# Performance work log

Measured on AMD Instinct MI355X. Metric: run time of the kernel, lower is better.

Reference implementation:

```python
import jax, jax.numpy as jnp
import numpy as np

B, NQ, NC, D, H, HD, FF, RB = 2, 512, 2048, 768, 12, 64, 3072, 64
EPS = 1e-5


def setup_inputs() -> dict:
    key = jax.random.key(0)
    ks = jax.random.split(key, 20)
    def n(k, shape, s=0.02):
        return jax.random.normal(k, shape, jnp.float32) * s
    return dict(
        query_state=n(ks[0], (B, NQ, D), 1.0),
        context_k=n(ks[1], (B, NC, D), 1.0),
        context_v=n(ks[2], (B, NC, D), 1.0),
        query_coords=jax.random.uniform(ks[3], (B, NQ, 2), jnp.float32),
        context_coords=jax.random.uniform(ks[4], (B, NC, 2), jnp.float32),
        sn_g=jnp.ones(D), sn_b=jnp.zeros(D),
        wqkv=n(ks[5], (D, 3 * D)), bqkv=jnp.zeros(3 * D),
        wo_s=n(ks[6], (D, D)), bo_s=jnp.zeros(D),
        cn_g=jnp.ones(D), cn_b=jnp.zeros(D),
        wq=n(ks[7], (D, D)), bq=jnp.zeros(D),
        wk=n(ks[8], (D, D)), bk=jnp.zeros(D),
        wv=n(ks[9], (D, D)), bv=jnp.zeros(D),
        wo_c=n(ks[10], (D, D)), bo_c=jnp.zeros(D),
        rb_w1=n(ks[11], (2, RB), 0.5), rb_b1=jnp.zeros(RB),
        rb_w2=n(ks[12], (RB, H), 0.5), rb_b2=jnp.zeros(H),
        fn_g=jnp.ones(D), fn_b=jnp.zeros(D),
        fw1=n(ks[13], (D, FF)), fb1=jnp.zeros(FF),
        fw2=n(ks[14], (FF, D)), fb2=jnp.zeros(D),
    )


def _ln(x, g, b):
    m = x.mean(-1, keepdims=True)
    v = ((x - m) ** 2).mean(-1, keepdims=True)
    return (x - m) / jnp.sqrt(v + EPS) * g + b


def _heads(x):
    # (B, N, D) -> (B, H, N, HD)
    return x.reshape(x.shape[0], x.shape[1], H, HD).transpose(0, 2, 1, 3)


def reference(query_state, context_k, context_v, query_coords, context_coords,
              sn_g, sn_b, wqkv, bqkv, wo_s, bo_s,
              cn_g, cn_b, wq, bq, wk, bk, wv, bv, wo_c, bo_c,
              rb_w1, rb_b1, rb_w2, rb_b2,
              fn_g, fn_b, fw1, fb1, fw2, fb2):
    scale = HD ** -0.5
    x = query_state

    # ---- pre-norm self-attention (nn.MultiheadAttention equivalent) ----
    qn = _ln(x, sn_g, sn_b)
    qkv = qn @ wqkv + bqkv                      # (B, NQ, 3D)
    q, k, v = jnp.split(qkv, 3, axis=-1)
    q, k, v = _heads(q), _heads(k), _heads(v)   # (B, H, NQ, HD)
    a = jax.nn.softmax(jnp.einsum('bhqd,bhkd->bhqk', q, k) * scale, axis=-1)
    o = jnp.einsum('bhqk,bhkd->bhqd', a, v).transpose(0, 2, 1, 3).reshape(B, NQ, D)
    x = x + o @ wo_s + bo_s

    # ---- relative coordinate bias: MLP(delta) -> (B, H, NQ, NC) ----
    delta = query_coords[:, :, None, :] - context_coords[:, None, :, :]  # (B, NQ, NC, 2)
    bias = jax.nn.gelu(delta @ rb_w1 + rb_b1, approximate=False) @ rb_w2 + rb_b2
    bias = bias.transpose(0, 3, 1, 2)           # (B, H, NQ, NC)

    # ---- pre-norm cross-attention with bias ----
    qn = _ln(x, cn_g, cn_b)
    q = _heads(qn @ wq + bq)                    # (B, H, NQ, HD)
    k = _heads(context_k @ wk + bk)             # (B, H, NC, HD)
    v = _heads(context_v @ wv + bv)
    logits = jnp.einsum('bhqd,bhkd->bhqk', q, k) * scale + bias
    a = jax.nn.softmax(logits, axis=-1)
    o = jnp.einsum('bhqk,bhkd->bhqd', a, v).transpose(0, 2, 1, 3).reshape(B, NQ, D)
    x = x + o @ wo_c + bo_c

    # ---- pre-norm FFN ----
    h = jax.nn.gelu(_ln(x, fn_g, fn_b) @ fw1 + fb1, approximate=False)
    x = x + h @ fw2 + fb2
    return x
```

## Files before the change

kernel.cpp:

```cpp
#include <hip/hip_runtime.h>

#define B_ 2
#define NQ_ 512
#define NC_ 2048
#define D_ 768
#define H_ 12
#define HD_ 64
#define FF_ 3072
#define RB_ 64

typedef unsigned short u16;
typedef __attribute__((ext_vector_type(4))) unsigned short u16x4;
typedef __attribute__((ext_vector_type(8))) short short8;
typedef __attribute__((ext_vector_type(4))) float f32x4;
typedef __attribute__((ext_vector_type(2))) float f32x2;

#define SCL2 0.18033688f

__device__ __forceinline__ float bf2f(u16 u) {
    unsigned int i = ((unsigned int)u) << 16;
    float f; __builtin_memcpy(&f, &i, 4); return f;
}
__device__ __forceinline__ u16 f2bf(float f) {
    unsigned int i; __builtin_memcpy(&i, &f, 4);
    unsigned int r = i + 0x7FFFu + ((i >> 16) & 1u);
    return (u16)(r >> 16);
}
__device__ __forceinline__ float gelu_f(float x) {
    return 0.5f * x * (1.f + erff(x * 0.70710678118654752f));
}
__device__ __forceinline__ float wsum(float v) {
    v += __shfl_xor(v, 32); v += __shfl_xor(v, 16); v += __shfl_xor(v, 8);
    v += __shfl_xor(v, 4);  v += __shfl_xor(v, 2);  v += __shfl_xor(v, 1);
    return v;
}
__device__ __forceinline__ void gload_lds16(const void* g, void* l) {
    __builtin_amdgcn_global_load_lds((const __attribute__((address_space(1))) void*)g,
                                     (__attribute__((address_space(3))) void*)l, 16, 0, 0);
}

__device__ __forceinline__ void wtrans_body(const float* __restrict__ in, u16* __restrict__ out,
                                            int K, int N, int bx, int by, int tid) {
    __shared__ float t[32][33];
    int n0 = bx * 32, k0 = by * 32;
    int tx = tid & 31, ty = tid >> 5;
#pragma unroll
    for (int r = 0; r < 4; ++r)
        t[ty + r * 8][tx] = in[(long)(k0 + ty + r * 8) * N + n0 + tx];
    __syncthreads();
#pragma unroll
    for (int r = 0; r < 4; ++r)
        out[(long)(n0 + ty + r * 8) * K + k0 + tx] = f2bf(t[tx][ty + r * 8]);
}

__global__ __launch_bounds__(256) void prep(
    const float* wqkv, u16* wT_qkv,
    const float* wo_s, const float* wq, const float* wk, const float* wv, const float* wo_c,
    u16* wT_os, u16* wT_q, u16* wT_k, u16* wT_v, u16* wT_oc,
    const float* fw1, u16* wT_f1, const float* fw2, u16* wT_f2,
    const float* ctx_k, u16* ckb, const float* ctx_v, u16* cvb,
    const float* bk, const float* bv, float* bkv) {
    int i = blockIdx.x, tid = threadIdx.x;
    if (i < 1728) { wtrans_body(wqkv, wT_qkv, 768, 2304, i % 72, i / 72, tid); return; }
    i -= 1728;
    if (i < 2880) {
        int z = i / 576, rem = i % 576;
        const float* in; u16* out;
        switch (z) {
            case 0: in = wo_s; out = wT_os; break;
            case 1: in = wq;   out = wT_q;  break;
            case 2: in = wk;   out = wT_k;  break;
            case 3: in = wv;   out = wT_v;  break;
            default: in = wo_c; out = wT_oc; break;
        }
        wtrans_body(in, out, 768, 768, rem % 24, rem / 24, tid);
        return;
    }
    i -= 2880;
    if (i < 2304) { wtrans_body(fw1, wT_f1, 768, 3072, i % 96, i / 96, tid); return; }
    i -= 2304;
    if (i < 2304) { wtrans_body(fw2, wT_f2, 3072, 768, i % 24, i / 24, tid); return; }
    i -= 2304;
    if (i < 6144) {
        int y = i / 3072;
        int ii = (i % 3072) * 256 + tid;
        const float* in = y ? ctx_v : ctx_k;
        u16* out = y ? cvb : ckb;
        float4 v = ((const float4*)in)[ii];
        u16x4 o; o.x = f2bf(v.x); o.y = f2bf(v.y); o.z = f2bf(v.z); o.w = f2bf(v.w);
        ((u16x4*)out)[ii] = o;
        return;
    }
    i -= 6144;
    {
        int j = i * 256 + tid;
        if (j < 768) bkv[j] = bk[j];
        else if (j < 1536) bkv[j] = bv[j - 768];
    }
}

__global__ __launch_bounds__(256) void ln_k(const float* __restrict__ x, const float* __restrict__ g,
                                            const float* __restrict__ bta, u16* __restrict__ out) {
    int row = blockIdx.x, t = threadIdx.x;
    const float* xr = x + (long)row * D_;
    float a0 = xr[t], a1 = xr[t + 256], a2 = xr[t + 512];
    float s = a0 + a1 + a2, s2 = a0 * a0 + a1 * a1 + a2 * a2;
    s = wsum(s); s2 = wsum(s2);
    __shared__ float rb[8];
    int lane = t & 63, wid = t >> 6;
    if (!lane) { rb[wid] = s; rb[wid + 4] = s2; }
    __syncthreads();
    float S = rb[0] + rb[1] + rb[2] + rb[3];
    float S2 = rb[4] + rb[5] + rb[6] + rb[7];
    float mean = S * (1.f / D_);
    float var = S2 * (1.f / D_) - mean * mean;
    float rstd = rsqrtf(var + 1e-5f);
    u16* orow = out + (long)row * D_;
    orow[t]       = f2bf((a0 - mean) * rstd * g[t]       + bta[t]);
    orow[t + 256] = f2bf((a1 - mean) * rstd * g[t + 256] + bta[t + 256]);
    orow[t + 512] = f2bf((a2 - mean) * rstd * g[t + 512] + bta[t + 512]);
}

#define BIAS_SMEM_BYTES (5888 + 12 * 264 * 2)
__device__ __forceinline__ void bias_body(char* smem,
    const float* __restrict__ qcoord, const float* __restrict__ ccoord,
    const float* __restrict__ w1, const float* __restrict__ b1,
    const float* __restrict__ w2, const float* __restrict__ b2,
    u16* __restrict__ out, int cx, int q4, int b, int tid) {
    float* s1 = (float*)smem;
    float* sw2 = (float*)(smem + 768);
    float2* sc = (float2*)(smem + 3840);
    u16* sb = (u16*)(smem + 5888);
    int q0 = q4 * 4, c0 = cx * 256;
    if (tid < 64) { s1[tid] = w1[tid]; s1[64 + tid] = w1[64 + tid]; s1[128 + tid] = b1[tid]; }
    for (int i = tid; i < RB_ * H_; i += 256) sw2[i] = w2[i];
    sc[tid] = ((const float2*)ccoord)[b * NC_ + c0 + tid];
    __syncthreads();
    int lane = tid & 63, wid = tid >> 6;
    int h = lane & 15, g4 = lane >> 4;
    int j0 = g4 * 8;
    f32x2 wx[8], wy[8], bb[8];
#pragma unroll
    for (int p = 0; p < 4; ++p) {
        wx[p]     = (f32x2){s1[j0 + 2 * p],       s1[j0 + 2 * p + 1]};
        wy[p]     = (f32x2){s1[64 + j0 + 2 * p],  s1[64 + j0 + 2 * p + 1]};
        bb[p]     = (f32x2){s1[128 + j0 + 2 * p], s1[128 + j0 + 2 * p + 1]};
        wx[4 + p] = (f32x2){s1[32 + j0 + 2 * p],  s1[32 + j0 + 2 * p + 1]};
        wy[4 + p] = (f32x2){s1[96 + j0 + 2 * p],  s1[96 + j0 + 2 * p + 1]};
        bb[4 + p] = (f32x2){s1[160 + j0 + 2 * p], s1[160 + j0 + 2 * p + 1]};
    }
    short8 vb0, vb1;
#pragma unroll
    for (int u = 0; u < 8; ++u) {
        vb0[u] = (h < 12) ? (short)f2bf(sw2[(j0 + u) * H_ + h]) : (short)0;
        vb1[u] = (h < 12) ? (short)f2bf(sw2[(32 + j0 + u) * H_ + h]) : (short)0;
    }
    float qx[4], qy[4];
#pragma unroll
    for (int qq = 0; qq < 4; ++qq) {
        qx[qq] = qcoord[(b * NQ_ + q0 + qq) * 2];
        qy[qq] = qcoord[(b * NQ_ + q0 + qq) * 2 + 1];
    }
    float b2v = (h < 12) ? b2[h] : 0.f;
#pragma unroll 1
    for (int qq = 0; qq < 4; ++qq) {
        if (qq) __syncthreads();
#pragma unroll
        for (int it = 0; it < 4; ++it) {
            int ci = wid * 64 + it * 16 + h;
            float2 cc = sc[ci];
            float dx = qx[qq] - cc.x, dy = qy[qq] - cc.y;
            unsigned int pk[8];
#pragma unroll
            for (int p = 0; p < 8; ++p) {
                f32x2 pre = dx * wx[p] + bb[p];
                pre = dy * wy[p] + pre;
                f32x2 xc = __builtin_elementwise_min(
                               __builtin_elementwise_max(pre, (f32x2)(-3.0f)), (f32x2)(3.0f));
                f32x2 u = xc * xc;
                f32x2 v = u * 2.3813e-5f + (-6.8939e-4f);
                v = v * u + 0.0086261f;
                v = v * u + (-0.064949f);
                v = v * u + 0.39837f;
                f32x2 phi = xc * v + 0.5f;
                f32x2 g = pre * phi;
                pk[p] = __builtin_amdgcn_perm(__builtin_bit_cast(unsigned int, g.y),
                                              __builtin_bit_cast(unsigned int, g.x), 0x07060302u);
            }
            uint4 d0 = {pk[0], pk[1], pk[2], pk[3]};
            uint4 d1 = {pk[4], pk[5], pk[6], pk[7]};
            short8 a0 = __builtin_bit_cast(short8, d0);
            short8 a1 = __builtin_bit_cast(short8, d1);
            f32x4 acc = {};
            acc = __builtin_amdgcn_mfma_f32_16x16x32_bf16(a0, vb0, acc, 0, 0, 0);
            acc = __builtin_amdgcn_mfma_f32_16x16x32_bf16(a1, vb1, acc, 0, 0, 0);
            if (h < 12) {
#pragma unroll
                for (int r = 0; r < 4; ++r) {
                    int loc = wid * 64 + it * 16 + g4 * 4 + r;
                    sb[h * 264 + loc] = f2bf((acc[r] + b2v) * 1.4426950f);
                }
            }
        }
        __syncthreads();
        for (int i = tid; i < 12 * 128; i += 256) {
            int row = i >> 7, cp = (i & 127) * 2;
            unsigned int pv = *(const unsigned int*)(sb + row * 264 + cp);
            *(unsigned int*)(out + (((long)(b * H_ + row) * NQ_ + q0 + qq) * NC_ + c0 + cp)) = pv;
        }
    }
}

__global__ __launch_bounds__(256) void vtrans(const u16* __restrict__ in, u16* __restrict__ out,
                                              int NCt, int ldin, int bdiv, long sIb, long sIh) {
    __shared__ u16 t[32][33];
    int z = blockIdx.z, zb = z / bdiv, zh = z % bdiv;
    const u16* ib = in + zb * sIb + zh * sIh;
    int c0 = blockIdx.x * 32, d0 = blockIdx.y * 32;
    int tx = threadIdx.x & 31, ty = threadIdx.x >> 5;
#pragma unroll
    for (int r = 0; r < 4; ++r)
        t[ty + r * 8][tx] = ib[(long)(c0 + ty + r * 8) * ldin + d0 + tx];
    __syncthreads();
#pragma unroll
    for (int r = 0; r < 4; ++r)
        out[(long)z * 64 * NCt + (long)(d0 + ty + r * 8) * NCt + c0 + tx] = t[tx][ty + r * 8];
}

template <int NCT, bool HASBIAS>
__global__ __launch_bounds__(64) void fattn(
    const u16* __restrict__ Qb, const u16* __restrict__ Kb, const u16* __restrict__ Vtb,
    const u16* __restrict__ Bias, u16* __restrict__ Ob, int ldq, int ldk) {
    __shared__ u16 kl[2][128 * 64];
    __shared__ u16 vl[64 * 128];
    __shared__ u16 pl[16 * 128];
    const int lane = threadIdx.x;
    const int h16 = lane & 15, g4 = lane >> 4;
    const int hh = blockIdx.y, b = blockIdx.z, q0 = blockIdx.x * 16;
    const u16* Qrow = Qb + (long)(b * NQ_ + q0 + h16) * ldq + hh * 64;
    short8 qf0 = *(const short8*)(Qrow + g4 * 8);
    short8 qf1 = *(const short8*)(Qrow + 32 + g4 * 8);
    const u16* Kbase = Kb + (long)b * NCT * ldk + hh * 64;
    const u16* Vtbase = Vtb + (long)(b * H_ + hh) * 64 * NCT;

    auto stageK = [&](int buf, int c0) {
#pragma unroll
        for (int i = 0; i < 16; ++i) {
            int ch = i * 64 + lane;
            int row = ch >> 3, col2 = (ch & 7) * 16;
            int scol2 = col2 ^ ((row & 7) << 4);
            gload_lds16(Kbase + (long)(c0 + row) * ldk + (scol2 >> 1), &kl[buf][ch * 8]);
        }
    };
    auto stageV = [&](int c0) {
#pragma unroll
        for (int i = 0; i < 16; ++i) {
            int ch = i * 64 + lane;
            int row = ch >> 4, col2 = (ch & 15) * 16;
            int scol2 = col2 ^ ((row & 15) << 4);
            gload_lds16(Vtbase + (long)row * NCT + c0 + (scol2 >> 1), &vl[ch * 8]);
        }
    };

    float m0[4] = {-1e30f, -1e30f, -1e30f, -1e30f};
    float l0[4] = {0.f, 0.f, 0.f, 0.f};
    f32x4 oacc[4] = {};
    constexpr int T = NCT / 128;
    stageK(0, 0);
    for (int t = 0; t < T; ++t) {
        const int c0 = t * 128, cur = t & 1;
        asm volatile("s_waitcnt lgkmcnt(0)" ::: "memory");
        stageV(c0);
        if (t + 1 < T) stageK(cur ^ 1, c0 + 128);
        if (t + 1 < T) asm volatile("s_waitcnt vmcnt(32)" ::: "memory");
        else           asm volatile("s_waitcnt vmcnt(16)" ::: "memory");
        f32x4 sacc[8] = {};
        const u16* klc = kl[cur];
        __builtin_amdgcn_s_setprio(1);
#pragma unroll
        for (int n = 0; n < 8; ++n) {
            int row = n * 16 + h16, swz = (row & 7) << 4;
#pragma unroll
            for (int ks = 0; ks < 2; ++ks) {
                short8 kf = *(const short8*)((const char*)klc + row * 128 + ((ks * 64 + g4 * 16) ^ swz));
                sacc[n] = __builtin_amdgcn_mfma_f32_16x16x32_bf16(ks ? qf1 : qf0, kf, sacc[n], 0, 0, 0);
            }
        }
        __builtin_amdgcn_s_setprio(0);
        if (t + 1 < T) asm volatile("s_waitcnt vmcnt(16)" ::: "memory");
        else           asm volatile("s_waitcnt vmcnt(0)" ::: "memory");
        float cr[4];
#pragma unroll
        for (int r = 0; r < 4; ++r) {
            float mx = -1e30f;
#pragma unroll
            for (int n = 0; n < 8; ++n) {
                float s = sacc[n][r] * SCL2;
                sacc[n][r] = s; mx = fmaxf(mx, s);
            }
            mx = fmaxf(mx, __shfl_xor(mx, 1)); mx = fmaxf(mx, __shfl_xor(mx, 2));
            mx = fmaxf(mx, __shfl_xor(mx, 4)); mx = fmaxf(mx, __shfl_xor(mx, 8));
            float mn = fmaxf(m0[r], mx);
            cr[r] = __builtin_amdgcn_exp2f(m0[r] - mn); m0[r] = mn;
            float sum = 0.f;
#pragma unroll
            for (int n = 0; n < 8; ++n) {
                float p = __builtin_amdgcn_exp2f(sacc[n][r] - mn); sacc[n][r] = p; sum += p;
            }
            sum += __shfl_xor(sum, 1); sum += __shfl_xor(sum, 2);
            sum += __shfl_xor(sum, 4); sum += __shfl_xor(sum, 8);
            l0[r] = l0[r] * cr[r] + sum;
        }
#pragma unroll
        for (int n = 0; n < 8; ++n)
#pragma unroll
            for (int r = 0; r < 4; ++r) {
                int q = g4 * 4 + r, c = n * 16 + h16;
                *(u16*)((char*)pl + q * 256 + ((c * 2) ^ (q << 4))) =
                    (u16)(__builtin_bit_cast(unsigned int, sacc[n][r]) >> 16);
            }
#pragma unroll
        for (int d = 0; d < 4; ++d) {
            f32x4 o = oacc[d];
            o[0] *= cr[0]; o[1] *= cr[1]; o[2] *= cr[2]; o[3] *= cr[3];
            oacc[d] = o;
        }
        short8 pf[4];
#pragma unroll
        for (int ks = 0; ks < 4; ++ks)
            pf[ks] = *(const short8*)((const char*)pl + h16 * 256 + ((ks * 64 + g4 * 16) ^ (h16 << 4)));
        __builtin_amdgcn_s_setprio(1);
#pragma unroll
        for (int d = 0; d < 4; ++d) {
            int row = d * 16 + h16, swzv = (row & 15) << 4;
#pragma unroll
            for (int ks = 0; ks < 4; ++ks) {
                short8 vf = *(const short8*)((const char*)vl + row * 256 + ((ks * 64 + g4 * 16) ^ swzv));
                oacc[d] = __builtin_amdgcn_mfma_f32_16x16x32_bf16(pf[ks], vf, oacc[d], 0, 0, 0);
            }
        }
        __builtin_amdgcn_s_setprio(0);
    }
    float inv[4];
#pragma unroll
    for (int r = 0; r < 4; ++r) inv[r] = 1.f / l0[r];
    u16* Orow = Ob + (long)(b * NQ_ + q0) * D_ + hh * 64;
#pragma unroll
    for (int d = 0; d < 4; ++d)
#pragma unroll
        for (int r = 0; r < 4; ++r)
            Orow[(long)(g4 * 4 + r) * D_ + d * 16 + h16] = f2bf(oacc[d][r] * inv[r]);
}

template <int T, int S>
__global__ __launch_bounds__(256) void fattn4(
    const u16* __restrict__ Qb, const u16* __restrict__ Kb, const u16* __restrict__ Vtb,
    const u16* __restrict__ Bias, float* __restrict__ Part,
    int ldq, int ldk, int ldv, int NCT) {
    __shared__ u16 kl[2][64 * 64];
    __shared__ u16 vl[64 * 64];
    __shared__ u16 bl[4][16 * 64];
    __shared__ u16 pl[4][16 * 64];
    const int tid = threadIdx.x, lane = tid & 63, wid = tid >> 6;
    const int h16 = lane & 15, g4 = lane >> 4;
    const int qb = blockIdx.x, hh = blockIdx.y;
    const int b = blockIdx.z / S, s = blockIdx.z % S;
    const int q0w = qb * 64 + wid * 16;
    const int cb = s * (T * 64);
    const u16* Qrow = Qb + (long)(b * NQ_ + q0w + h16) * ldq + hh * 64;
    short8 qf0 = *(const short8*)(Qrow + g4 * 8);
    short8 qf1 = *(const short8*)(Qrow + 32 + g4 * 8);
    const u16* Kbase = Kb + (long)b * NCT * ldk + hh * 64;
    const u16* Vtbase = Vtb + (long)(b * H_ + hh) * 64 * ldv;
    const u16* Bbase = Bias + ((long)(b * H_ + hh) * NQ_ + q0w) * NCT;
    u16* mypl = pl[wid];
    const u16* mybl = bl[wid];

    auto stageK = [&](int buf, int c0) {
#pragma unroll
        for (int i = 0; i < 2; ++i) {
            int ch = wid * 128 + i * 64 + lane;
            int row = ch >> 3, col2 = (ch & 7) * 16;
            int scol2 = col2 ^ ((row & 7) << 4);
            gload_lds16(Kbase + (long)(c0 + row) * ldk + (scol2 >> 1), &kl[buf][ch * 8]);
        }
    };
    auto stageV = [&](int c0) {
#pragma unroll
        for (int i = 0; i < 2; ++i) {
            int ch = wid * 128 + i * 64 + lane;
            int row = ch >> 3, col2 = (ch & 7) * 16;
            int scol2 = col2 ^ ((row & 7) << 4);
            gload_lds16(Vtbase + (long)row * ldv + c0 + (scol2 >> 1), &vl[ch * 8]);
        }
    };
    auto stageB = [&](int c0) {
#pragma unroll
        for (int i = 0; i < 2; ++i) {
            int ch = i * 64 + lane;
            int row = ch >> 3, c16 = ch & 7;
            int sc16 = c16 ^ (row & 7);
            gload_lds16(Bbase + (long)row * NCT + c0 + sc16 * 8, &bl[wid][ch * 8]);
        }
    };

    float m0[4] = {-1e30f, -1e30f, -1e30f, -1e30f};
    float l0[4] = {0.f, 0.f, 0.f, 0.f};
    f32x4 oacc[4] = {};
    stageK(0, cb);
    for (int t = 0; t < T; ++t) {
        const int c0 = cb + t * 64, cur = t & 1;
        if (t > 0) {
            asm volatile("s_waitcnt lgkmcnt(0)" ::: "memory");
            __builtin_amdgcn_sched_barrier(0);
            __builtin_amdgcn_s_barrier();
        }
        stageV(c0);
        stageB(c0);
        if (t + 1 < T) stageK(cur ^ 1, c0 + 64);
        if (t + 1 < T) asm volatile("s_waitcnt vmcnt(6)" ::: "memory");
        else           asm volatile("s_waitcnt vmcnt(4)" ::: "memory");
        __builtin_amdgcn_s_barrier();
        f32x4 sacc[4] = {};
        const u16* klc = kl[cur];
        __builtin_amdgcn_s_setprio(1);
#pragma unroll
        for (int n = 0; n < 4; ++n) {
            int row = n * 16 + h16, swz = (row & 7) << 4;
#pragma unroll
            for (int ks = 0; ks < 2; ++ks) {
                short8 kf = *(const short8*)((const char*)klc + row * 128 + ((ks * 64 + g4 * 16) ^ swz));
                sacc[n] = __builtin_amdgcn_mfma_f32_16x16x32_bf16(ks ? qf1 : qf0, kf, sacc[n], 0, 0, 0);
            }
        }
        __builtin_amdgcn_s_setprio(0);
        if (t + 1 < T) asm volatile("s_waitcnt vmcnt(2)" ::: "memory");
        else           asm volatile("s_waitcnt vmcnt(0)" ::: "memory");
        __builtin_amdgcn_s_barrier();
        float cr[4];
#pragma unroll
        for (int r = 0; r < 4; ++r) {
            int q = g4 * 4 + r;
            float mx = -1e30f;
#pragma unroll
            for (int n = 0; n < 4; ++n) {
                float bvv = bf2f(*(const u16*)((const char*)mybl + q * 128 +
                                 (((n * 16 + h16) * 2) ^ ((q & 7) << 4))));
                float sv = sacc[n][r] * SCL2 + bvv;
                sacc[n][r] = sv; mx = fmaxf(mx, sv);
            }
            mx = fmaxf(mx, __shfl_xor(mx, 1)); mx = fmaxf(mx, __shfl_xor(mx, 2));
            mx = fmaxf(mx, __shfl_xor(mx, 4)); mx = fmaxf(mx, __shfl_xor(mx, 8));
            float mn = fmaxf(m0[r], mx);
            cr[r] = __builtin_amdgcn_exp2f(m0[r] - mn); m0[r] = mn;
            float sum = 0.f;
#pragma unroll
            for (int n = 0; n < 4; ++n) {
                float p = __builtin_amdgcn_exp2f(sacc[n][r] - mn); sacc[n][r] = p; sum += p;
            }
            sum += __shfl_xor(sum, 1); sum += __shfl_xor(sum, 2);
            sum += __shfl_xor(sum, 4); sum += __shfl_xor(sum, 8);
            l0[r] = l0[r] * cr[r] + sum;
        }
#pragma unroll
        for (int n = 0; n < 4; ++n)
#pragma unroll
            for (int r = 0; r < 4; ++r) {
                int q = g4 * 4 + r, c = n * 16 + h16;
                *(u16*)((char*)mypl + q * 128 + ((c * 2) ^ ((q & 7) << 4))) =
                    (u16)(__builtin_bit_cast(unsigned int, sacc[n][r]) >> 16);
            }
#pragma unroll
        for (int d = 0; d < 4; ++d) {
            f32x4 o = oacc[d];
            o[0] *= cr[0]; o[1] *= cr[1]; o[2] *= cr[2]; o[3] *= cr[3];
            oacc[d] = o;
        }
        short8 pf[2];
#pragma unroll
        for (int ks = 0; ks < 2; ++ks)
            pf[ks] = *(const short8*)((const char*)mypl + h16 * 128 + ((ks * 64 + g4 * 16) ^ ((h16 & 7) << 4)));
        __builtin_amdgcn_s_setprio(1);
#pragma unroll
        for (int d = 0; d < 4; ++d) {
            int row = d * 16 + h16, swzv = (row & 7) << 4;
#pragma unroll
            for (int ks = 0; ks < 2; ++ks) {
                short8 vf = *(const short8*)((const char*)vl + row * 128 + ((ks * 64 + g4 * 16) ^ swzv));
                oacc[d] = __builtin_amdgcn_mfma_f32_16x16x32_bf16(pf[ks], vf, oacc[d], 0, 0, 0);
            }
        }
        __builtin_amdgcn_s_setprio(0);
    }
    float* P = Part + ((((long)(b * H_ + hh) * 32 + qb * 4 + wid) * S + s) * 1088);
#pragma unroll
    for (int d = 0; d < 4; ++d)
#pragma unroll
        for (int r = 0; r < 4; ++r)
            P[(g4 * 4 + r) * 64 + d * 16 + h16] = oacc[d][r];
    if (h16 == 0) {
#pragma unroll
        for (int r = 0; r < 4; ++r) {
            P[1024 + g4 * 4 + r] = m0[r];
            P[1056 + g4 * 4 + r] = l0[r];
        }
    }
}

__global__ __launch_bounds__(64) void fcomb(const float* __restrict__ Part, u16* __restrict__ Ob) {
    int q16 = blockIdx.x, hh = blockIdx.y, b = blockIdx.z, lane = threadIdx.x;
    const float* base = Part + (((long)(b * H_ + hh) * 32 + q16) * 4) * 1088;
#pragma unroll 4
    for (int q = 0; q < 16; ++q) {
        float m0 = base[1024 + q],        m1 = base[1088 + 1024 + q];
        float m2 = base[2176 + 1024 + q], m3 = base[3264 + 1024 + q];
        float M = fmaxf(fmaxf(m0, m1), fmaxf(m2, m3));
        float w0 = __builtin_amdgcn_exp2f(m0 - M), w1 = __builtin_amdgcn_exp2f(m1 - M);
        float w2 = __builtin_amdgcn_exp2f(m2 - M), w3 = __builtin_amdgcn_exp2f(m3 - M);
        float L = w0 * base[1056 + q] + w1 * base[1088 + 1056 + q] +
                  w2 * base[2176 + 1056 + q] + w3 * base[3264 + 1056 + q];
        float o = w0 * base[q * 64 + lane] + w1 * base[1088 + q * 64 + lane] +
                  w2 * base[2176 + q * 64 + lane] + w3 * base[3264 + q * 64 + lane];
        Ob[(long)(b * NQ_ + q16 * 16 + q) * D_ + hh * 64 + lane] = f2bf(o * (1.f / L));
    }
}

enum { EP_BIAS = 0, EP_SCALE = 1, EP_RES = 3, EP_GELU = 4 };

template <int BM, int BN, int EPI>
__device__ __forceinline__ void gemm_body(
    u16* lA, u16* lB,
    const u16* __restrict__ A, const u16* __restrict__ B, void* __restrict__ Cv,
    const float* __restrict__ bias, const float* __restrict__ res,
    int M, int N, int K, int lda, int ldb, int ldc,
    int bdiv, long sAb, long sAh, long sBb, long sBh, long sCb, long sCh,
    float scale, int biasz, int bx, int by, int z, int tid) {
    constexpr int BK = 64;
    const int zb = z / bdiv, zh = z % bdiv;
    const u16* Ab = A + zb * sAb + zh * sAh;
    const u16* Bb = B + zb * sBb + zh * sBh;
    const int bm = by * BM;
    const int bn = bx * BN;
    const int lane = tid & 63, wid = tid >> 6;
    const int wm = (wid >> 1) * (BM / 2);
    const int wn = (wid & 1) * (BN / 2);
    constexpr int FM = BM / 32, FN = BN / 32;
    f32x4 acc[FM][FN] = {};
    const int lrow = lane & 15, lk = (lane >> 4) * 8;

    for (int kb = 0; kb < K; kb += BK) {
#pragma unroll
        for (int i = 0; i < (BM * 8) / 256; ++i) {
            int ch = tid + i * 256;
            int r = ch >> 3, c = ch & 7;
            gload_lds16(Ab + (long)(bm + r) * lda + kb + c * 8, lA + ch * 8);
        }
#pragma unroll
        for (int i = 0; i < (BN * 8) / 256; ++i) {
            int ch = tid + i * 256;
            int r = ch >> 3, c = ch & 7;
            gload_lds16(Bb + (long)(bn + r) * ldb + kb + c * 8, lB + ch * 8);
        }
        __syncthreads();
#pragma unroll
        for (int ks = 0; ks < 2; ++ks) {
            short8 af[FM], bfr[FN];
#pragma unroll
            for (int i = 0; i < FM; ++i)
                af[i] = *(const short8*)(lA + (wm + i * 16 + lrow) * BK + ks * 32 + lk);
#pragma unroll
            for (int j = 0; j < FN; ++j)
                bfr[j] = *(const short8*)(lB + (wn + j * 16 + lrow) * BK + ks * 32 + lk);
#pragma unroll
            for (int i = 0; i < FM; ++i)
#pragma unroll
                for (int j = 0; j < FN; ++j)
                    acc[i][j] = __builtin_amdgcn_mfma_f32_16x16x32_bf16(af[i], bfr[j], acc[i][j], 0, 0, 0);
        }
        __syncthreads();
    }

    long coff = zb * sCb + zh * sCh;
#pragma unroll
    for (int i = 0; i < FM; ++i) {
#pragma unroll
        for (int j = 0; j < FN; ++j) {
#pragma unroll
            for (int r = 0; r < 4; ++r) {
                int row = bm + wm + i * 16 + (lane >> 4) * 4 + r;
                int col = bn + wn + j * 16 + (lane & 15);
                long idx = coff + (long)row * ldc + col;
                float v = acc[i][j][r];
                if (EPI == EP_SCALE) {
                    ((u16*)Cv)[idx] = f2bf(v * scale);
                } else if (EPI == EP_RES) {
                    float tt = v + (bias ? bias[col] : 0.f);
                    ((float*)Cv)[idx] = res[idx] + tt;
                } else if (EPI == EP_GELU) {
                    float tt = v + (bias ? bias[col] : 0.f);
                    ((u16*)Cv)[idx] = f2bf(gelu_f(tt));
                } else {
                    float tt = v + (bias ? bias[biasz * zb + col] : 0.f);
                    ((u16*)Cv)[idx] = f2bf(tt);
                }
            }
        }
    }
}

template <int BM, int BN, int EPI>
__global__ __launch_bounds__(256) void gemm_bt(
    const u16* __restrict__ A, const u16* __restrict__ B, void* __restrict__ Cv,
    const float* __restrict__ bias, const float* __restrict__ res,
    int M, int N, int K, int lda, int ldb, int ldc,
    int bdiv, long sAb, long sAh, long sBb, long sBh, long sCb, long sCh,
    float scale, int biasz) {
    __shared__ u16 lA[BM * 64];
    __shared__ u16 lB[BN * 64];
    gemm_body<BM, BN, EPI>(lA, lB, A, B, Cv, bias, res, M, N, K, lda, ldb, ldc,
                           bdiv, sAb, sAh, sBb, sBh, sCb, sCh, scale, biasz,
                           blockIdx.x, blockIdx.y, blockIdx.z, threadIdx.x);
}

__global__ __launch_bounds__(256) void kvproj_bias(
    const u16* __restrict__ ckb, const u16* __restrict__ wT_k, u16* __restrict__ kc,
    const float* __restrict__ bkv,
    const float* __restrict__ qcoord, const float* __restrict__ ccoord,
    const float* __restrict__ rb_w1, const float* __restrict__ rb_b1,
    const float* __restrict__ rb_w2, const float* __restrict__ rb_b2,
    u16* __restrict__ clog) {
    __shared__ __attribute__((aligned(16))) char smem[(64 + 128) * 64 * 2];
    int idx = blockIdx.x, tid = threadIdx.x;
    if (idx < 768) {
        int z = idx / 384, rem = idx % 384;
        int bx = rem % 6, by = rem / 6;
        gemm_body<64, 128, EP_BIAS>((u16*)smem, (u16*)(smem + 64 * 64 * 2),
            ckb, wT_k, kc, bkv, nullptr, 4096, 768, 768, 768, 768, 768,
            1, (long)B_ * NC_ * D_, 0, (long)768 * 768, 0, (long)4096 * 768, 0,
            1.f, 768, bx, by, z, tid);
    } else {
        int bidx = idx - 768;
        int cx = bidx & 7, q4 = (bidx >> 3) & 127, b = bidx >> 10;
        bias_body(smem, qcoord, ccoord, rb_w1, rb_b1, rb_w2, rb_b2, clog, cx, q4, b, tid);
    }
}

extern "C" void kernel_launch(void* const* d_in, const int* in_sizes, int n_in,
                              void* d_out, int out_size, void* d_ws, size_t ws_size,
                              hipStream_t stream) {
    const float* x_in   = (const float*)d_in[0];
    const float* ctx_k  = (const float*)d_in[1];
    const float* ctx_v  = (const float*)d_in[2];
    const float* qcoord = (const float*)d_in[3];
    const float* ccoord = (const float*)d_in[4];
    const float* sn_g   = (const float*)d_in[5];
    const float* sn_b   = (const float*)d_in[6];
    const float* wqkv   = (const float*)d_in[7];
    const float* bqkv   = (const float*)d_in[8];
    const float* wo_s   = (const float*)d_in[9];
    const float* bo_s   = (const float*)d_in[10];
    const float* cn_g   = (const float*)d_in[11];
    const float* cn_b   = (const float*)d_in[12];
    const float* wq     = (const float*)d_in[13];
    const float* bq     = (const float*)d_in[14];
    const float* wk     = (const float*)d_in[15];
    const float* bk     = (const float*)d_in[16];
    const float* wv     = (const float*)d_in[17];
    const float* bv     = (const float*)d_in[18];
    const float* wo_c   = (const float*)d_in[19];
    const float* bo_c   = (const float*)d_in[20];
    const float* rb_w1  = (const float*)d_in[21];
    const float* rb_b1  = (const float*)d_in[22];
    const float* rb_w2  = (const float*)d_in[23];
    const float* rb_b2  = (const float*)d_in[24];
    const float* fn_g   = (const float*)d_in[25];
    const float* fn_b   = (const float*)d_in[26];
    const float* fw1    = (const float*)d_in[27];
    const float* fb1    = (const float*)d_in[28];
    const float* fw2    = (const float*)d_in[29];
    const float* fb2    = (const float*)d_in[30];

    char* ws = (char*)d_ws;
    size_t off = 0;
    auto alloc = [&](size_t bytes) -> void* {
        void* p = ws + off; off += (bytes + 255) & ~(size_t)255; return p;
    };
    u16* wT_qkv = (u16*)alloc((size_t)2304 * 768 * 2);
    u16* wT_os  = (u16*)alloc((size_t)768 * 768 * 2);
    u16* wT_q   = (u16*)alloc((size_t)768 * 768 * 2);
    u16* wT_k   = (u16*)alloc((size_t)768 * 768 * 2);
    u16* wT_v   = (u16*)alloc((size_t)768 * 768 * 2);
    u16* wT_oc  = (u16*)alloc((size_t)768 * 768 * 2);
    u16* wT_f1  = (u16*)alloc((size_t)3072 * 768 * 2);
    u16* wT_f2  = (u16*)alloc((size_t)768 * 3072 * 2);
    u16* ckb    = (u16*)alloc((size_t)B_ * NC_ * D_ * 2);
    u16* cvb    = (u16*)alloc((size_t)B_ * NC_ * D_ * 2);
    u16* xln    = (u16*)alloc((size_t)1024 * 768 * 2);
    u16* qkv    = (u16*)alloc((size_t)1024 * 2304 * 2);
    u16* vts    = (u16*)alloc((size_t)24 * 64 * 512 * 2);
    u16* oatt   = (u16*)alloc((size_t)1024 * 768 * 2);
    float* x1   = (float*)alloc((size_t)1024 * 768 * 4);
    u16* xln2   = (u16*)alloc((size_t)1024 * 768 * 2);
    u16* qc     = (u16*)alloc((size_t)1024 * 768 * 2);
    u16* kc     = (u16*)alloc((size_t)4096 * 768 * 2);
    u16* vc     = (u16*)alloc((size_t)4096 * 768 * 2);
    u16* clog   = (u16*)alloc((size_t)24 * 512 * 2048 * 2);
    u16* vtc    = (u16*)alloc((size_t)24 * 64 * 2048 * 2);
    u16* oc2    = (u16*)alloc((size_t)1024 * 768 * 2);
    float* x2   = (float*)alloc((size_t)1024 * 768 * 4);
    u16* xln3   = (u16*)alloc((size_t)1024 * 768 * 2);
    u16* ffh    = (u16*)alloc((size_t)1024 * 3072 * 2);
    float* part = (float*)alloc((size_t)2 * H_ * 32 * 4 * 1088 * 4);
    float* bkv  = (float*)alloc((size_t)1536 * 4);
    (void)ws_size; (void)in_sizes; (void)n_in; (void)out_size;

    prep<<<15366, 256, 0, stream>>>(wqkv, wT_qkv, wo_s, wq, wk, wv, wo_c,
                                    wT_os, wT_q, wT_k, wT_v, wT_oc,
                                    fw1, wT_f1, fw2, wT_f2,
                                    ctx_k, ckb, ctx_v, cvb, bk, bv, bkv);

    ln_k<<<1024, 256, 0, stream>>>(x_in, sn_g, sn_b, xln);
    gemm_bt<64, 128, EP_BIAS><<<dim3(2304 / 128, 1024 / 64, 1), 256, 0, stream>>>(
        xln, wT_qkv, qkv, bqkv, nullptr, 1024, 2304, 768, 768, 768, 2304,
        1, 0, 0, 0, 0, 0, 0, 1.f, 0);
    vtrans<<<dim3(512 / 32, 2, 24), 256, 0, stream>>>(qkv + 1536, vts, 512, 2304, 12, (long)512 * 2304, 64);
    fattn<512, false><<<dim3(NQ_ / 16, H_, B_), 64, 0, stream>>>(
        qkv, qkv + 768, vts, nullptr, oatt, 2304, 2304);
    gemm_bt<32, 64, EP_RES><<<dim3(768 / 64, 1024 / 32, 1), 256, 0, stream>>>(
        oatt, wT_os, x1, bo_s, x_in, 1024, 768, 768, 768, 768, 768,
        1, 0, 0, 0, 0, 0, 0, 1.f, 0);

    ln_k<<<1024, 256, 0, stream>>>(x1, cn_g, cn_b, xln2);
    gemm_bt<32, 64, EP_BIAS><<<dim3(768 / 64, 1024 / 32, 1), 256, 0, stream>>>(
        xln2, wT_q, qc, bq, nullptr, 1024, 768, 768, 768, 768, 768,
        1, 0, 0, 0, 0, 0, 0, 1.f, 0);
    kvproj_bias<<<2816, 256, 0, stream>>>(ckb, wT_k, kc, bkv,
                                          qcoord, ccoord, rb_w1, rb_b1, rb_w2, rb_b2, clog);
    vtrans<<<dim3(2048 / 32, 2, 24), 256, 0, stream>>>(vc, vtc, 2048, 768, 12, (long)2048 * 768, 64);
    fattn4<8, 4><<<dim3(8, H_, B_ * 4), 256, 0, stream>>>(
        qc, kc, vtc, clog, part, 768, 768, 2048, 2048);
    fcomb<<<dim3(32, H_, B_), 64, 0, stream>>>(part, oc2);
    gemm_bt<32, 64, EP_RES><<<dim3(768 / 64, 1024 / 32, 1), 256, 0, stream>>>(
        oc2, wT_oc, x2, bo_c, x1, 1024, 768, 768, 768, 768, 768,
        1, 0, 0, 0, 0, 0, 0, 1.f, 0);

    ln_k<<<1024, 256, 0, stream>>>(x2, fn_g, fn_b, xln3);
    gemm_bt<64, 128, EP_GELU><<<dim3(3072 / 128, 1024 / 64, 1), 256, 0, stream>>>(
        xln3, wT_f1, ffh, fb1, nullptr, 1024, 3072, 768, 768, 768, 3072,
        1, 0, 0, 0, 0, 0, 0, 1.f, 0);
    gemm_bt<32, 64, EP_RES><<<dim3(768 / 64, 1024 / 32, 1), 256, 0, stream>>>(
        ffh, wT_f2, (float*)d_out, fb2, x2, 1024, 768, 3072, 3072, 3072, 768,
        1, 0, 0, 0, 0, 0, 0, 1.f, 0);
}
```

Measured before the change: 242.0 us.

## Split fused K-projection/bias kernel and shrink GEMM tiles for QKV and FFN1

The combined kvproj_bias launch is split into a standalone bias MLP kernel and a separate K-projection GEMM. The bias kernel is moved earlier, right after the QKV GEMM, so it no longer shares a launch with the K GEMM. The QKV and FFN-up GEMMs switch from 64x128 to 32x64 tiles, which gives more workgroups to fill the CUs. The trade-off is less data reuse per tile and one extra kernel launch.

```diff
diff --git a/kernel.cpp b/kernel.cpp
--- a/kernel.cpp
+++ b/kernel.cpp
@@ -121,17 +121,17 @@
     orow[t + 512] = f2bf((a2 - mean) * rstd * g[t + 512] + bta[t + 512]);
 }
 
-#define BIAS_SMEM_BYTES (5888 + 12 * 264 * 2)
-__device__ __forceinline__ void bias_body(char* smem,
+__global__ __launch_bounds__(256) void bias_mlp7(
     const float* __restrict__ qcoord, const float* __restrict__ ccoord,
     const float* __restrict__ w1, const float* __restrict__ b1,
     const float* __restrict__ w2, const float* __restrict__ b2,
-    u16* __restrict__ out, int cx, int q4, int b, int tid) {
-    float* s1 = (float*)smem;
-    float* sw2 = (float*)(smem + 768);
-    float2* sc = (float2*)(smem + 3840);
-    u16* sb = (u16*)(smem + 5888);
-    int q0 = q4 * 4, c0 = cx * 256;
+    u16* __restrict__ out) {
+    __shared__ float s1[192];
+    __shared__ float sw2[RB_ * H_];
+    __shared__ float2 sc[256];
+    __shared__ u16 sb[12 * 264];
+    int tid = threadIdx.x;
+    int b = blockIdx.z, q0 = blockIdx.y * 4, c0 = blockIdx.x * 256;
     if (tid < 64) { s1[tid] = w1[tid]; s1[64 + tid] = w1[64 + tid]; s1[128 + tid] = b1[tid]; }
     for (int i = tid; i < RB_ * H_; i += 256) sw2[i] = w2[i];
     sc[tid] = ((const float2*)ccoord)[b * NC_ + c0 + tid];
@@ -528,19 +528,22 @@
 enum { EP_BIAS = 0, EP_SCALE = 1, EP_RES = 3, EP_GELU = 4 };
 
 template <int BM, int BN, int EPI>
-__device__ __forceinline__ void gemm_body(
-    u16* lA, u16* lB,
+__global__ __launch_bounds__(256) void gemm_bt(
     const u16* __restrict__ A, const u16* __restrict__ B, void* __restrict__ Cv,
     const float* __restrict__ bias, const float* __restrict__ res,
     int M, int N, int K, int lda, int ldb, int ldc,
     int bdiv, long sAb, long sAh, long sBb, long sBh, long sCb, long sCh,
-    float scale, int biasz, int bx, int by, int z, int tid) {
+    float scale, int biasz) {
     constexpr int BK = 64;
+    __shared__ u16 lA[BM * BK];
+    __shared__ u16 lB[BN * BK];
+    const int z = blockIdx.z;
     const int zb = z / bdiv, zh = z % bdiv;
     const u16* Ab = A + zb * sAb + zh * sAh;
     const u16* Bb = B + zb * sBb + zh * sBh;
-    const int bm = by * BM;
-    const int bn = bx * BN;
+    const int bm = blockIdx.y * BM;
+    const int bn = blockIdx.x * BN;
+    const int tid = threadIdx.x;
     const int lane = tid & 63, wid = tid >> 6;
     const int wm = (wid >> 1) * (BM / 2);
     const int wn = (wid & 1) * (BN / 2);
@@ -605,43 +608,6 @@
                 }
             }
         }
-    }
-}
-
-template <int BM, int BN, int EPI>
-__global__ __launch_bounds__(256) void gemm_bt(
-    const u16* __restrict__ A, const u16* __restrict__ B, void* __restrict__ Cv,
-    const float* __restrict__ bias, const float* __restrict__ res,
-    int M, int N, int K, int lda, int ldb, int ldc,
-    int bdiv, long sAb, long sAh, long sBb, long sBh, long sCb, long sCh,
-    float scale, int biasz) {
-    __shared__ u16 lA[BM * 64];
-    __shared__ u16 lB[BN * 64];
-    gemm_body<BM, BN, EPI>(lA, lB, A, B, Cv, bias, res, M, N, K, lda, ldb, ldc,
-                           bdiv, sAb, sAh, sBb, sBh, sCb, sCh, scale, biasz,
-                           blockIdx.x, blockIdx.y, blockIdx.z, threadIdx.x);
-}
-
-__global__ __launch_bounds__(256) void kvproj_bias(
-    const u16* __restrict__ ckb, const u16* __restrict__ wT_k, u16* __restrict__ kc,
-    const float* __restrict__ bkv,
-    const float* __restrict__ qcoord, const float* __restrict__ ccoord,
-    const float* __restrict__ rb_w1, const float* __restrict__ rb_b1,
-    const float* __restrict__ rb_w2, const float* __restrict__ rb_b2,
-    u16* __restrict__ clog) {
-    __shared__ __attribute__((aligned(16))) char smem[(64 + 128) * 64 * 2];
-    int idx = blockIdx.x, tid = threadIdx.x;
-    if (idx < 768) {
-        int z = idx / 384, rem = idx % 384;
-        int bx = rem % 6, by = rem / 6;
-        gemm_body<64, 128, EP_BIAS>((u16*)smem, (u16*)(smem + 64 * 64 * 2),
-            ckb, wT_k, kc, bkv, nullptr, 4096, 768, 768, 768, 768, 768,
-            1, (long)B_ * NC_ * D_, 0, (long)768 * 768, 0, (long)4096 * 768, 0,
-            1.f, 768, bx, by, z, tid);
-    } else {
-        int bidx = idx - 768;
-        int cx = bidx & 7, q4 = (bidx >> 3) & 127, b = bidx >> 10;
-        bias_body(smem, qcoord, ccoord, rb_w1, rb_b1, rb_w2, rb_b2, clog, cx, q4, b, tid);
     }
 }
 
@@ -720,9 +686,10 @@
                                     ctx_k, ckb, ctx_v, cvb, bk, bv, bkv);
 
     ln_k<<<1024, 256, 0, stream>>>(x_in, sn_g, sn_b, xln);
-    gemm_bt<64, 128, EP_BIAS><<<dim3(2304 / 128, 1024 / 64, 1), 256, 0, stream>>>(
+    gemm_bt<32, 64, EP_BIAS><<<dim3(2304 / 64, 1024 / 32, 1), 256, 0, stream>>>(
         xln, wT_qkv, qkv, bqkv, nullptr, 1024, 2304, 768, 768, 768, 2304,
         1, 0, 0, 0, 0, 0, 0, 1.f, 0);
+    bias_mlp7<<<dim3(NC_ / 256, NQ_ / 4, B_), 256, 0, stream>>>(qcoord, ccoord, rb_w1, rb_b1, rb_w2, rb_b2, clog);
     vtrans<<<dim3(512 / 32, 2, 24), 256, 0, stream>>>(qkv + 1536, vts, 512, 2304, 12, (long)512 * 2304, 64);
     fattn<512, false><<<dim3(NQ_ / 16, H_, B_), 64, 0, stream>>>(
         qkv, qkv + 768, vts, nullptr, oatt, 2304, 2304);
@@ -734,8 +701,9 @@
     gemm_bt<32, 64, EP_BIAS><<<dim3(768 / 64, 1024 / 32, 1), 256, 0, stream>>>(
         xln2, wT_q, qc, bq, nullptr, 1024, 768, 768, 768, 768, 768,
         1, 0, 0, 0, 0, 0, 0, 1.f, 0);
-    kvproj_bias<<<2816, 256, 0, stream>>>(ckb, wT_k, kc, bkv,
-                                          qcoord, ccoord, rb_w1, rb_b1, rb_w2, rb_b2, clog);
+    gemm_bt<64, 128, EP_BIAS><<<dim3(768 / 128, 4096 / 64, 2), 256, 0, stream>>>(
+        ckb, wT_k, kc, bkv, nullptr, 4096, 768, 768, 768, 768, 768,
+        1, (long)B_ * NC_ * D_, 0, (long)768 * 768, 0, (long)4096 * 768, 0, 1.f, 768);
     vtrans<<<dim3(2048 / 32, 2, 24), 256, 0, stream>>>(vc, vtc, 2048, 768, 12, (long)2048 * 768, 64);
     fattn4<8, 4><<<dim3(8, H_, B_ * 4), 256, 0, stream>>>(
         qc, kc, vtc, clog, part, 768, 768, 2048, 2048);
@@ -745,7 +713,7 @@
         1, 0, 0, 0, 0, 0, 0, 1.f, 0);
 
     ln_k<<<1024, 256, 0, stream>>>(x2, fn_g, fn_b, xln3);
-    gemm_bt<64, 128, EP_GELU><<<dim3(3072 / 128, 1024 / 64, 1), 256, 0, stream>>>(
+    gemm_bt<32, 64, EP_GELU><<<dim3(3072 / 64, 1024 / 32, 1), 256, 0, stream>>>(
         xln3, wT_f1, ffh, fb1, nullptr, 1024, 3072, 768, 768, 768, 3072,
         1, 0, 0, 0, 0, 0, 0, 1.f, 0);
     gemm_bt<32, 64, EP_RES><<<dim3(768 / 64, 1024 / 32, 1), 256, 0, stream>>>(
```

Result: no change. 239.1 us (-1.2%).
